# Kernel optimization log

Measured on AMD Instinct MI355X. Metric: run time of the kernel, lower is better.

Reference implementation:

```python
import jax, jax.numpy as jnp
import numpy as np

K, T, V = 64, 100, 10000
DELTA = 0.005
EPS_DIV = 1e-6


def setup_inputs() -> dict:
    key = jax.random.key(0)
    k1, k2, k3 = jax.random.split(key, 3)
    mu_q_beta = jax.random.normal(k1, (K, T, V), dtype=jnp.float32)
    logsig_q_beta = jax.random.normal(k2, (K, T, V), dtype=jnp.float32)
    eps = jax.random.normal(k3, (T, K, V), dtype=jnp.float32)  # randn_like noise for reparameterize
    return {"mu_q_beta": mu_q_beta, "logsig_q_beta": logsig_q_beta, "eps": eps}


def reference(mu_q_beta, logsig_q_beta, eps):
    # Rearrange params from [K, T, V] to the time-major layout [T, K, V]
    mu = jnp.transpose(mu_q_beta, (1, 0, 2))
    ls = jnp.transpose(logsig_q_beta, (1, 0, 2))

    # reparameterize: beta[t] = mu[t] + exp(0.5 * logsig[t]) * eps[t]
    # (beta[t] has no dependency on beta[t-1] -> fully vectorized over T)
    betas = mu + jnp.exp(0.5 * ls) * eps  # [T, K, V]

    # KL at t=0 against N(0, I): p_logsigma = 0 -> sigma_p_sq = 1
    kl0 = 0.5 * jnp.sum((jnp.exp(ls[0]) + mu[0] ** 2) / (1.0 + EPS_DIV) - 1.0 - ls[0])

    # KL at t>=1 against N(beta[t-1], delta): sigma_p_sq = delta, p_logsigma = log(delta)
    log_delta = jnp.log(jnp.float32(DELTA))
    diff = mu[1:] - betas[:-1]  # one-step lag prior mean
    kl_rest = 0.5 * jnp.sum(
        (jnp.exp(ls[1:]) + diff ** 2) / (DELTA + EPS_DIV) - 1.0 + log_delta - ls[1:]
    )

    kl_beta = kl0 + kl_rest
    return jax.nn.softmax(betas, axis=-1), kl_beta
```

## Files before the change

kernel.cpp:

```cpp
#include <hip/hip_runtime.h>
#include <math.h>

#define KDIM 64
#define TDIM 100
#define VDIM 10000
#define NV4  2500
#define BLOCK 512
#define NWAVE (BLOCK / 64)
#define VPT 5
#define CHUNK 5
#define NCHUNK (TDIM / CHUNK)

#define INV1 (1.0f / (1.0f + 1e-6f))
#define INVD (1.0f / (0.005f + 1e-6f))
#define LOGD (-5.2983173665480363f)

typedef float vf4 __attribute__((ext_vector_type(4)));

#define INRANGE(jj, idx) ((jj) < VPT - 1 || (idx) < NV4)

__device__ __forceinline__ float wave_red_sum(float v) {
#pragma unroll
    for (int m = 32; m >= 1; m >>= 1) v += __shfl_xor(v, m, 64);
    return v;
}

__device__ __forceinline__ void lds_barrier() {
    asm volatile("s_waitcnt lgkmcnt(0)\n\ts_barrier" ::: "memory");
}

__global__ __launch_bounds__(BLOCK, 4) void fused_beta_softmax_kl(
    const float* __restrict__ mu_q,
    const float* __restrict__ lsq,
    const float* __restrict__ eps,
    float* __restrict__ out,
    float* __restrict__ kl)
{
    __shared__ vf4 bprev[NV4];
    __shared__ float red[2][NWAVE];
    __shared__ float kred[NWAVE];

    const int tid = threadIdx.x;
    const int bid = blockIdx.x;
    const int k   = bid / NCHUNK;
    const int c   = bid % NCHUNK;
    const int t0  = c * CHUNK;
    const int tend = t0 + CHUNK;
    const bool epi = (tend < TDIM);

    float klacc = 0.0f;
    vf4 M[VPT], L[VPT], E[VPT];

    for (int t = t0; t < tend; ++t) {
        const size_t po = ((size_t)k * TDIM + t) * VDIM;
        const size_t eo = ((size_t)t * KDIM + k) * VDIM;
        const vf4* m4p = reinterpret_cast<const vf4*>(mu_q + po);
        const vf4* l4p = reinterpret_cast<const vf4*>(lsq + po);
        const vf4* e4p = reinterpret_cast<const vf4*>(eps + eo);
        const bool first = (t == 0);
        const bool skip  = (t == t0) && (t0 != 0);

#pragma unroll
        for (int jj = 0; jj < VPT; ++jj) {
            const int idx = tid + jj * BLOCK;
            if (INRANGE(jj, idx)) {
                M[jj] = m4p[idx];
                L[jj] = l4p[idx];
                E[jj] = __builtin_nontemporal_load(&e4p[idx]);
            }
        }

        float lsum = 0.0f;
#pragma unroll
        for (int jj = 0; jj < VPT; ++jj) {
            const int idx = tid + jj * BLOCK;
            if (INRANGE(jj, idx)) {
                const vf4 m = M[jj], l = L[jj], e = E[jj];
                vf4 b;
                b.x = fmaf(__expf(0.5f * l.x), e.x, m.x);
                b.y = fmaf(__expf(0.5f * l.y), e.y, m.y);
                b.z = fmaf(__expf(0.5f * l.z), e.z, m.z);
                b.w = fmaf(__expf(0.5f * l.w), e.w, m.w);
                if (first) {
                    klacc += (__expf(l.x) + m.x * m.x) * INV1 - 1.0f - l.x;
                    klacc += (__expf(l.y) + m.y * m.y) * INV1 - 1.0f - l.y;
                    klacc += (__expf(l.z) + m.z * m.z) * INV1 - 1.0f - l.z;
                    klacc += (__expf(l.w) + m.w * m.w) * INV1 - 1.0f - l.w;
                } else if (!skip) {
                    const vf4 p = bprev[idx];
                    const float dx = m.x - p.x, dy = m.y - p.y,
                                dz = m.z - p.z, dw = m.w - p.w;
                    klacc += (__expf(l.x) + dx * dx) * INVD - 1.0f + LOGD - l.x;
                    klacc += (__expf(l.y) + dy * dy) * INVD - 1.0f + LOGD - l.y;
                    klacc += (__expf(l.z) + dz * dz) * INVD - 1.0f + LOGD - l.z;
                    klacc += (__expf(l.w) + dw * dw) * INVD - 1.0f + LOGD - l.w;
                }
                bprev[idx] = b;
                lsum += __expf(b.x) + __expf(b.y) + __expf(b.z) + __expf(b.w);
            }
        }

        const int slot = t & 1;
        float ws = wave_red_sum(lsum);
        if ((tid & 63) == 0) red[slot][tid >> 6] = ws;
        lds_barrier();
        float rowsum = 0.0f;
#pragma unroll
        for (int w = 0; w < NWAVE; ++w) rowsum += red[slot][w];
        const float invs = 1.0f / rowsum;

        vf4* o4p = reinterpret_cast<vf4*>(out + ((size_t)t * KDIM + k) * VDIM);
#pragma unroll
        for (int jj = 0; jj < VPT; ++jj) {
            const int idx = tid + jj * BLOCK;
            if (INRANGE(jj, idx)) {
                const vf4 b = bprev[idx];
                vf4 o;
                o.x = __expf(b.x) * invs;
                o.y = __expf(b.y) * invs;
                o.z = __expf(b.z) * invs;
                o.w = __expf(b.w) * invs;
                __builtin_nontemporal_store(o, &o4p[idx]);
            }
        }
    }

    if (epi) {
        const size_t po = ((size_t)k * TDIM + tend) * VDIM;
        const vf4* m4p = reinterpret_cast<const vf4*>(mu_q + po);
        const vf4* l4p = reinterpret_cast<const vf4*>(lsq + po);
#pragma unroll
        for (int jj = 0; jj < VPT; ++jj) {
            const int idx = tid + jj * BLOCK;
            if (INRANGE(jj, idx)) { M[jj] = m4p[idx]; L[jj] = l4p[idx]; }
        }
#pragma unroll
        for (int jj = 0; jj < VPT; ++jj) {
            const int idx = tid + jj * BLOCK;
            if (INRANGE(jj, idx)) {
                const vf4 m = M[jj], l = L[jj];
                const vf4 p = bprev[idx];
                const float dx = m.x - p.x, dy = m.y - p.y,
                            dz = m.z - p.z, dw = m.w - p.w;
                klacc += (__expf(l.x) + dx * dx) * INVD - 1.0f + LOGD - l.x;
                klacc += (__expf(l.y) + dy * dy) * INVD - 1.0f + LOGD - l.y;
                klacc += (__expf(l.z) + dz * dz) * INVD - 1.0f + LOGD - l.z;
                klacc += (__expf(l.w) + dw * dw) * INVD - 1.0f + LOGD - l.w;
            }
        }
    }

    float wk = wave_red_sum(klacc);
    __syncthreads();
    if ((tid & 63) == 0) kred[tid >> 6] = wk;
    __syncthreads();
    if (tid == 0) {
        float tot = 0.0f;
#pragma unroll
        for (int w = 0; w < NWAVE; ++w) tot += kred[w];
        atomicAdd(kl, 0.5f * tot);
    }
}

extern "C" void kernel_launch(void* const* d_in, const int* in_sizes, int n_in,
                              void* d_out, int out_size, void* d_ws, size_t ws_size,
                              hipStream_t stream) {
    const float* mu_q = (const float*)d_in[0];
    const float* lsq  = (const float*)d_in[1];
    const float* eps  = (const float*)d_in[2];
    float* out = (float*)d_out;
    float* kl  = out + (size_t)TDIM * KDIM * VDIM;

    (void)hipMemsetAsync(kl, 0, sizeof(float), stream);

    dim3 grid(KDIM * NCHUNK);
    fused_beta_softmax_kl<<<grid, BLOCK, 0, stream>>>(mu_q, lsq, eps, out, kl);
}
```

Before: 200.7 us.

## Prefetch next timestep inputs before softmax phase and reuse sqrt-sigma exp

Loads for timestep t+1 (mu, logsig, eps) and the epilogue's lookahead row are now issued right after the beta/KL compute for timestep t, before the reduction barrier and output store phase. This lets global memory latency overlap with the softmax normalization and stores. It also computes exp(0.5*l) once and squares it for the KL term instead of issuing a second exp. The kernel is memory-bound, so the prefetch overlap is the main intent. It keeps register use the same because it reuses the M/L/E arrays.

New measurement: 205.9 us. 2.6% more time.

```diff
diff --git a/kernel.cpp b/kernel.cpp
--- a/kernel.cpp
+++ b/kernel.cpp
@@ -51,15 +51,12 @@
     float klacc = 0.0f;
     vf4 M[VPT], L[VPT], E[VPT];
 
-    for (int t = t0; t < tend; ++t) {
-        const size_t po = ((size_t)k * TDIM + t) * VDIM;
-        const size_t eo = ((size_t)t * KDIM + k) * VDIM;
+    {
+        const size_t po = ((size_t)k * TDIM + t0) * VDIM;
+        const size_t eo = ((size_t)t0 * KDIM + k) * VDIM;
         const vf4* m4p = reinterpret_cast<const vf4*>(mu_q + po);
         const vf4* l4p = reinterpret_cast<const vf4*>(lsq + po);
         const vf4* e4p = reinterpret_cast<const vf4*>(eps + eo);
-        const bool first = (t == 0);
-        const bool skip  = (t == t0) && (t0 != 0);
-
 #pragma unroll
         for (int jj = 0; jj < VPT; ++jj) {
             const int idx = tid + jj * BLOCK;
@@ -69,6 +66,11 @@
                 E[jj] = __builtin_nontemporal_load(&e4p[idx]);
             }
         }
+    }
+
+    for (int t = t0; t < tend; ++t) {
+        const bool first = (t == 0);
+        const bool skip  = (t == t0) && (t0 != 0);
 
         float lsum = 0.0f;
 #pragma unroll
@@ -76,27 +78,55 @@
             const int idx = tid + jj * BLOCK;
             if (INRANGE(jj, idx)) {
                 const vf4 m = M[jj], l = L[jj], e = E[jj];
+                const float sx = __expf(0.5f * l.x), sy = __expf(0.5f * l.y),
+                            sz = __expf(0.5f * l.z), sw = __expf(0.5f * l.w);
                 vf4 b;
-                b.x = fmaf(__expf(0.5f * l.x), e.x, m.x);
-                b.y = fmaf(__expf(0.5f * l.y), e.y, m.y);
-                b.z = fmaf(__expf(0.5f * l.z), e.z, m.z);
-                b.w = fmaf(__expf(0.5f * l.w), e.w, m.w);
+                b.x = fmaf(sx, e.x, m.x);
+                b.y = fmaf(sy, e.y, m.y);
+                b.z = fmaf(sz, e.z, m.z);
+                b.w = fmaf(sw, e.w, m.w);
                 if (first) {
-                    klacc += (__expf(l.x) + m.x * m.x) * INV1 - 1.0f - l.x;
-                    klacc += (__expf(l.y) + m.y * m.y) * INV1 - 1.0f - l.y;
-                    klacc += (__expf(l.z) + m.z * m.z) * INV1 - 1.0f - l.z;
-                    klacc += (__expf(l.w) + m.w * m.w) * INV1 - 1.0f - l.w;
+                    klacc += (sx * sx + m.x * m.x) * INV1 - 1.0f - l.x;
+                    klacc += (sy * sy + m.y * m.y) * INV1 - 1.0f - l.y;
+                    klacc += (sz * sz + m.z * m.z) * INV1 - 1.0f - l.z;
+                    klacc += (sw * sw + m.w * m.w) * INV1 - 1.0f - l.w;
                 } else if (!skip) {
                     const vf4 p = bprev[idx];
                     const float dx = m.x - p.x, dy = m.y - p.y,
                                 dz = m.z - p.z, dw = m.w - p.w;
-                    klacc += (__expf(l.x) + dx * dx) * INVD - 1.0f + LOGD - l.x;
-                    klacc += (__expf(l.y) + dy * dy) * INVD - 1.0f + LOGD - l.y;
-                    klacc += (__expf(l.z) + dz * dz) * INVD - 1.0f + LOGD - l.z;
-                    klacc += (__expf(l.w) + dw * dw) * INVD - 1.0f + LOGD - l.w;
+                    klacc += (sx * sx + dx * dx) * INVD - 1.0f + LOGD - l.x;
+                    klacc += (sy * sy + dy * dy) * INVD - 1.0f + LOGD - l.y;
+                    klacc += (sz * sz + dz * dz) * INVD - 1.0f + LOGD - l.z;
+                    klacc += (sw * sw + dw * dw) * INVD - 1.0f + LOGD - l.w;
                 }
                 bprev[idx] = b;
                 lsum += __expf(b.x) + __expf(b.y) + __expf(b.z) + __expf(b.w);
+            }
+        }
+
+        if (t + 1 < tend) {
+            const size_t po = ((size_t)k * TDIM + (t + 1)) * VDIM;
+            const size_t eo = ((size_t)(t + 1) * KDIM + k) * VDIM;
+            const vf4* m4p = reinterpret_cast<const vf4*>(mu_q + po);
+            const vf4* l4p = reinterpret_cast<const vf4*>(lsq + po);
+            const vf4* e4p = reinterpret_cast<const vf4*>(eps + eo);
+#pragma unroll
+            for (int jj = 0; jj < VPT; ++jj) {
+                const int idx = tid + jj * BLOCK;
+                if (INRANGE(jj, idx)) {
+                    M[jj] = m4p[idx];
+                    L[jj] = l4p[idx];
+                    E[jj] = __builtin_nontemporal_load(&e4p[idx]);
+                }
+            }
+        } else if (epi) {
+            const size_t po = ((size_t)k * TDIM + tend) * VDIM;
+            const vf4* m4p = reinterpret_cast<const vf4*>(mu_q + po);
+            const vf4* l4p = reinterpret_cast<const vf4*>(lsq + po);
+#pragma unroll
+            for (int jj = 0; jj < VPT; ++jj) {
+                const int idx = tid + jj * BLOCK;
+                if (INRANGE(jj, idx)) { M[jj] = m4p[idx]; L[jj] = l4p[idx]; }
             }
         }
 
@@ -126,26 +156,20 @@
     }
 
     if (epi) {
-        const size_t po = ((size_t)k * TDIM + tend) * VDIM;
-        const vf4* m4p = reinterpret_cast<const vf4*>(mu_q + po);
-        const vf4* l4p = reinterpret_cast<const vf4*>(lsq + po);
-#pragma unroll
-        for (int jj = 0; jj < VPT; ++jj) {
-            const int idx = tid + jj * BLOCK;
-            if (INRANGE(jj, idx)) { M[jj] = m4p[idx]; L[jj] = l4p[idx]; }
-        }
 #pragma unroll
         for (int jj = 0; jj < VPT; ++jj) {
             const int idx = tid + jj * BLOCK;
             if (INRANGE(jj, idx)) {
                 const vf4 m = M[jj], l = L[jj];
                 const vf4 p = bprev[idx];
+                const float sx = __expf(0.5f * l.x), sy = __expf(0.5f * l.y),
+                            sz = __expf(0.5f * l.z), sw = __expf(0.5f * l.w);
                 const float dx = m.x - p.x, dy = m.y - p.y,
                             dz = m.z - p.z, dw = m.w - p.w;
-                klacc += (__expf(l.x) + dx * dx) * INVD - 1.0f + LOGD - l.x;
-                klacc += (__expf(l.y) + dy * dy) * INVD - 1.0f + LOGD - l.y;
-                klacc += (__expf(l.z) + dz * dz) * INVD - 1.0f + LOGD - l.z;
-                klacc += (__expf(l.w) + dw * dw) * INVD - 1.0f + LOGD - l.w;
+                klacc += (sx * sx + dx * dx) * INVD - 1.0f + LOGD - l.x;
+                klacc += (sy * sy + dy * dy) * INVD - 1.0f + LOGD - l.y;
+                klacc += (sz * sz + dz * dz) * INVD - 1.0f + LOGD - l.z;
+                klacc += (sw * sw + dw * dw) * INVD - 1.0f + LOGD - l.w;
             }
         }
     }
```
